# Optimization experiments

Hardware: AMD Instinct MI355X
Metric: run time of the kernel (lower is better)

Reference implementation:

```python
import jax, jax.numpy as jnp
import numpy as np
import math

D = 256
NH = 4
MULT = 128
N = MULT * D // NH  # 8192
N_LAYER = 6
VOCAB = 256
THETA = 2 ** 16
EPS = 1e-5


def get_freqs(n):
    ar = jnp.arange(n, dtype=jnp.float32)
    q = jnp.floor(ar / 2.0) * 2.0  # quantize in pairs
    return 1.0 / (THETA ** (q / n)) / (2.0 * math.pi)


def layer_norm(x):
    m = jnp.mean(x, axis=-1, keepdims=True)
    v = jnp.var(x, axis=-1, keepdims=True)
    return (x - m) / jnp.sqrt(v + EPS)


def rope_apply(v, cos, sin):
    # interleaved rotation: v_rot = stack((-v[odd], v[even])) interleaved back
    v_rot = jnp.stack([-v[..., 1::2], v[..., ::2]], axis=-1).reshape(v.shape)
    return v * cos + v_rot * sin


def setup_inputs() -> dict:
    key = jax.random.key(0)
    ks = jax.random.split(key, 6)
    idx = jax.random.randint(ks[0], (1, 1024), 0, VOCAB)
    embed = jax.random.normal(ks[1], (VOCAB, D), dtype=jnp.float32) * 0.02
    encoder = jax.random.normal(ks[2], (NH, D, N), dtype=jnp.float32) * 0.02
    encoder_v = jax.random.normal(ks[3], (NH, D, N), dtype=jnp.float32) * 0.02
    decoder = jax.random.normal(ks[4], (NH * N, D), dtype=jnp.float32) * 0.02
    lm_head = jax.random.normal(ks[5], (D, VOCAB), dtype=jnp.float32) * 0.02
    return {"idx": idx, "embed": embed, "encoder": encoder,
            "encoder_v": encoder_v, "decoder": decoder, "lm_head": lm_head}


def reference(idx, embed, encoder, encoder_v, decoder, lm_head):
    B, T = idx.shape
    x = layer_norm(embed[idx])  # (B, T, D)

    freqs = get_freqs(N)  # (N,)
    phases = (jnp.arange(T, dtype=jnp.float32)[:, None] * freqs[None, :]) % 1.0
    phases = phases * (2.0 * math.pi)
    cos = jnp.cos(phases)[None, None]  # (1,1,T,N)
    sin = jnp.sin(phases)[None, None]

    causal = jnp.tril(jnp.ones((T, T), dtype=jnp.float32), k=-1)  # strict lower

    for _ in range(N_LAYER):
        # x_sparse: (B, nh, T, N)
        x_sparse = jax.nn.relu(jnp.einsum('btd,hdn->bhtn', x, encoder))
        QR = rope_apply(x_sparse, cos, sin)
        # raw (no-softmax) strictly-causal attention, V = x broadcast over heads
        scores = jnp.einsum('bhtn,bhsn->bhts', QR, QR) * causal
        yKV = layer_norm(jnp.einsum('bhts,bsd->bhtd', scores, x))
        y_sparse = jax.nn.relu(jnp.einsum('bhtd,hdn->bhtn', yKV, encoder_v))
        xy = x_sparse * y_sparse  # (B, nh, T, N)
        # head-major flatten then project back to D
        yMLP = xy.transpose(0, 2, 1, 3).reshape(B, T, NH * N) @ decoder
        y = layer_norm(yMLP)
        x = layer_norm(x + y)

    logits = x @ lm_head  # (B, T, VOCAB)
    return logits
```

## Files before the change

kernel.cpp:

```cpp
#include <hip/hip_runtime.h>
#include <math.h>


typedef __bf16 bf16;
typedef bf16  bf16x2 __attribute__((ext_vector_type(2)));
typedef bf16  bf16x8 __attribute__((ext_vector_type(8)));
typedef float f32x4  __attribute__((ext_vector_type(4)));

#define BM 128
#define BN 128
#define BK 32
#define SW 32

typedef __attribute__((address_space(3))) unsigned int lds_uint;
typedef const __attribute__((address_space(1))) unsigned int glb_uint;

__device__ __forceinline__ void ld_g2l16(const void* g, void* l) {
  __builtin_amdgcn_global_load_lds((glb_uint*)g, (lds_uint*)l, 16, 0, 0);
}

__device__ __forceinline__ float block_sum256(float v) {
  __shared__ float sb[4];
#pragma unroll
  for (int o = 32; o > 0; o >>= 1) v += __shfl_down(v, o);
  __syncthreads();
  if ((threadIdx.x & 63) == 0) sb[threadIdx.x >> 6] = v;
  __syncthreads();
  return sb[0] + sb[1] + sb[2] + sb[3];
}

template <int MODE>
__global__ __launch_bounds__(256) void gemm_bt(
    const bf16* __restrict__ A, long lda, long aZ, long aZ2,
    const bf16* __restrict__ Bt, long ldb, long bZ, long bZ2,
    void* __restrict__ Cv, long ldc, long cZ,
    void* __restrict__ Dv, long dZ,
    int M, int N, int K) {
  int m0, n0;
  long z = blockIdx.z;
  if (MODE == 6) {
    const int combo = blockIdx.x;
    const int tile  = blockIdx.y;
    const int tr = (int)((sqrtf(8.f * tile + 1.f) - 1.f) * 0.5f);
    const int tc = tile - tr * (tr + 1) / 2;
    m0 = tr * BM; n0 = tc * BN;
    A  += (long)(combo >> 3) * aZ2 + (long)(combo & 7) * aZ;
    Bt += (long)(combo >> 3) * bZ2 + (long)(combo & 7) * bZ;
  } else if (MODE == 7) {
    const int combo = blockIdx.x;
    z = combo;
    m0 = (blockIdx.y >> 1) * BM;
    n0 = (blockIdx.y & 1) * BN;
    A  += (combo & 7) * aZ + (combo >> 3) * aZ2;
    Bt += (combo & 7) * bZ + (combo >> 3) * bZ2;
  } else {
    m0 = blockIdx.y * BM;
    n0 = blockIdx.x * BN;
    if (MODE == 2 && n0 > m0) return;
    A  += (z & 3) * aZ + (z >> 2) * aZ2;
    Bt += (z & 3) * bZ + (z >> 2) * bZ2;
  }

  __shared__ __align__(16) bf16 As[2][BM * SW];
  __shared__ __align__(16) bf16 Bs[2][BN * SW];

  const int tid  = threadIdx.x;
  const int lane = tid & 63;
  const int wr   = (tid >> 6) >> 1;
  const int wc   = (tid >> 6) & 1;
  const int l15  = lane & 15;
  const int qd   = lane >> 4;

  f32x4 acc[4][4] = {};

  int Keff = K;
  if (MODE == 3) { int kc = m0 + BM; Keff = kc < K ? kc : K; }

  const int srow = tid >> 2;
  const int skc  = (tid & 3) * 8;
  const bf16* ap = A + (long)(m0 + srow) * lda + skc;
  const bf16* bp = Bt + (long)(n0 + srow) * ldb + skc;

  auto stage = [&](int buf, int k0) {
    char* AsB = (char*)&As[buf][0];
    char* BsB = (char*)&Bs[buf][0];
    ld_g2l16(ap + k0,            AsB + tid * 16);
    ld_g2l16(ap + k0 + 64 * lda, AsB + 4096 + tid * 16);
    ld_g2l16(bp + k0,            BsB + tid * 16);
    ld_g2l16(bp + k0 + 64 * ldb, BsB + 4096 + tid * 16);
  };
  auto compute = [&](int buf) {
    bf16x8 af[4], bfr[4];
#pragma unroll
    for (int i = 0; i < 4; i++)
      af[i] = *(const bf16x8*)&As[buf][(wr * 64 + i * 16 + l15) * SW + qd * 8];
#pragma unroll
    for (int j = 0; j < 4; j++)
      bfr[j] = *(const bf16x8*)&Bs[buf][(wc * 64 + j * 16 + l15) * SW + qd * 8];
#pragma unroll
    for (int i = 0; i < 4; i++)
#pragma unroll
      for (int j = 0; j < 4; j++)
        acc[i][j] = __builtin_amdgcn_mfma_f32_16x16x32_bf16(af[i], bfr[j], acc[i][j], 0, 0, 0);
  };

  stage(0, 0);
  __syncthreads();
  int cur = 0;
  for (int k0 = BK; k0 < Keff; k0 += BK) {
    stage(cur ^ 1, k0);
    compute(cur);
    __syncthreads();
    cur ^= 1;
  }
  compute(cur);

#pragma unroll
  for (int i = 0; i < 4; i++) {
#pragma unroll
    for (int j = 0; j < 4; j++) {
#pragma unroll
      for (int r = 0; r < 4; r++) {
        const int row = m0 + wr * 64 + i * 16 + qd * 4 + r;
        const int col = n0 + wc * 64 + j * 16 + l15;
        float v = acc[i][j][r];
        if (MODE == 1) {
          float rv = fmaxf(v, 0.f);
          float pv = __shfl_xor(rv, 1);
          ((bf16*)Cv)[z * cZ + (long)row * ldc + col] = (bf16)rv;
          float freq = exp2f(-(float)(col >> 1) * (1.0f / 256.0f)) * 0.15915494309189535f;
          float ph = (float)row * freq;
          ph -= floorf(ph);
          float s, c;
          __sincosf(ph * 6.283185307179586f, &s, &c);
          float rot = (col & 1) ? pv : -pv;
          ((bf16*)Dv)[z * dZ + (long)row * ldc + col] = (bf16)(rv * c + rot * s);
        } else if (MODE == 2) {
          ((bf16*)Cv)[z * cZ + (long)row * ldc + col] = (bf16)((col < row) ? v : 0.f);
        } else if (MODE == 4) {
          float rv = fmaxf(v, 0.f);
          float xv = (float)((const bf16*)Dv)[z * dZ + (long)row * 8192 + col];
          ((bf16*)Cv)[z * cZ + (long)row * ldc + col] = (bf16)(rv * xv);
        } else if (MODE == 6) {
          const int combo = blockIdx.x;
          long base = (((long)(combo & 7) * 4 + (combo >> 3)) * 36 + blockIdx.y) * 16384;
          ((bf16*)Cv)[base + (long)(row - m0) * 128 + (col - n0)] = (bf16)v;
        } else {
          ((float*)Cv)[z * cZ + (long)row * ldc + col] = v;
        }
      }
    }
  }
}

__global__ void reduce_sc(const bf16* __restrict__ scpart, bf16* __restrict__ sc) {
  const int tile = blockIdx.x >> 2, q = blockIdx.x & 3, head = blockIdx.y;
  const int tr = (int)((sqrtf(8.f * tile + 1.f) - 1.f) * 0.5f);
  const int tc = tile - tr * (tr + 1) / 2;
  const long t0p = ((long)head * 589824 + (long)tile * 16384) >> 1;
  const bf16x2* sp = (const bf16x2*)scpart;
  for (int p = q * 2048 + threadIdx.x; p < q * 2048 + 2048; p += 256) {
    float s0 = 0.f, s1 = 0.f;
#pragma unroll
    for (int s = 0; s < 8; s++) {
      bf16x2 v = sp[(long)s * 1179648 + t0p + p];
      s0 += (float)v.x; s1 += (float)v.y;
    }
    int i = p * 2;
    int lr = i >> 7, lc = i & 127;
    int grow = tr * 128 + lr, gcol = tc * 128 + lc;
    bf16x2 o;
    o.x = (bf16)((gcol < grow) ? s0 : 0.f);
    o.y = (bf16)((gcol + 1 < grow) ? s1 : 0.f);
    *(bf16x2*)&sc[(long)head * 1048576 + (long)grow * 1024 + gcol] = o;
  }
}

__global__ void transpose_cvt(const float* __restrict__ in, bf16* __restrict__ out,
                              int R, int C, long inZ, long outZ) {
  in += (long)blockIdx.z * inZ;
  out += (long)blockIdx.z * outZ;
  __shared__ float tile[32][33];
  int c0 = blockIdx.x * 32, r0 = blockIdx.y * 32;
  int lc = threadIdx.x & 31, lr8 = threadIdx.x >> 5;
#pragma unroll
  for (int i = 0; i < 32; i += 8)
    tile[lr8 + i][lc] = in[(long)(r0 + lr8 + i) * C + c0 + lc];
  __syncthreads();
#pragma unroll
  for (int i = 0; i < 32; i += 8)
    out[(long)(c0 + lr8 + i) * R + r0 + lc] = (bf16)tile[lc][lr8 + i];
}

__global__ void embed_ln(const int* __restrict__ idx, const float* __restrict__ embed,
                         float* __restrict__ x, bf16* __restrict__ xb,
                         bf16* __restrict__ xT) {
  int t = blockIdx.x, d = threadIdx.x;
  float v = embed[(long)idx[t] * 256 + d];
  float m = block_sum256(v) * (1.0f / 256.0f);
  float c = v - m;
  float var = block_sum256(c * c) * (1.0f / 256.0f);
  float o = c * rsqrtf(var + 1e-5f);
  x[t * 256 + d] = o;
  xb[t * 256 + d] = (bf16)o;
  xT[d * 1024 + t] = (bf16)o;
}

__global__ void ln_rows(const float* __restrict__ in, bf16* __restrict__ out) {
  int r = blockIdx.x, d = threadIdx.x;
  float v = in[(long)r * 256 + d];
  float m = block_sum256(v) * (1.0f / 256.0f);
  float c = v - m;
  float var = block_sum256(c * c) * (1.0f / 256.0f);
  out[(long)r * 256 + d] = (bf16)(c * rsqrtf(var + 1e-5f));
}

__global__ void ln_fuse(const float* __restrict__ part, float* __restrict__ x,
                        bf16* __restrict__ xb, bf16* __restrict__ xT) {
  int t = blockIdx.x, d = threadIdx.x;
  float s = 0.f;
#pragma unroll
  for (int i = 0; i < 32; i++) s += part[(long)i * 262144 + t * 256 + d];
  float m = block_sum256(s) * (1.0f / 256.0f);
  float c = s - m;
  float var = block_sum256(c * c) * (1.0f / 256.0f);
  float y = c * rsqrtf(var + 1e-5f);
  float zv = x[t * 256 + d] + y;
  m = block_sum256(zv) * (1.0f / 256.0f);
  c = zv - m;
  var = block_sum256(c * c) * (1.0f / 256.0f);
  float o = c * rsqrtf(var + 1e-5f);
  x[t * 256 + d] = o;
  xb[t * 256 + d] = (bf16)o;
  xT[d * 1024 + t] = (bf16)o;
}

extern "C" void kernel_launch(void* const* d_in, const int* in_sizes, int n_in,
                              void* d_out, int out_size, void* d_ws, size_t ws_size,
                              hipStream_t stream) {
  const int*   idx = (const int*)d_in[0];
  const float* emb = (const float*)d_in[1];
  float* out = (float*)d_out;
  char* ws  = (char*)d_ws;

  bf16*  encT   = (bf16*)(ws + 0L);
  bf16*  encvT  = (bf16*)(ws + 16777216L);
  bf16*  decT   = (bf16*)(ws + 33554432L);
  bf16*  lmT    = (bf16*)(ws + 50331648L);
  float* x      = (float*)(ws + 50462720L);
  bf16*  xb     = (bf16*)(ws + 51511296L);
  bf16*  xT     = (bf16*)(ws + 52035584L);
  bf16*  xs     = (bf16*)(ws + 52559872L);
  bf16*  qr     = (bf16*)(ws + 119668736L);
  bf16*  sc     = (bf16*)(ws + 186777600L);
  bf16*  scpart = (bf16*)(ws + 195166208L);
  float* ykv    = (float*)(ws + 195166208L);
  bf16*  ykvln  = (bf16*)(ws + 199360512L);
  float* part   = (float*)(ws + 195166208L);
  const bool big = ws_size >= 232914944UL;

  transpose_cvt<<<dim3(256, 8, 4), dim3(256), 0, stream>>>((const float*)d_in[2], encT, 256, 8192, 2097152L, 2097152L);
  transpose_cvt<<<dim3(256, 8, 4), dim3(256), 0, stream>>>((const float*)d_in[3], encvT, 256, 8192, 2097152L, 2097152L);
  transpose_cvt<<<dim3(8, 1024, 1), dim3(256), 0, stream>>>((const float*)d_in[4], decT, 32768, 256, 0L, 0L);
  transpose_cvt<<<dim3(8, 8, 1), dim3(256), 0, stream>>>((const float*)d_in[5], lmT, 256, 256, 0L, 0L);
  embed_ln<<<dim3(1024), dim3(256), 0, stream>>>(idx, emb, x, xb, xT);

  for (int l = 0; l < 6; l++) {
    gemm_bt<1><<<dim3(64, 8, 4), dim3(256), 0, stream>>>(
        xb, 256L, 0L, 0L, encT, 256L, 2097152L, 8388608L,
        (void*)xs, 8192L, 8388608L, (void*)qr, 8388608L, 1024, 8192, 256);
    if (big) {
      gemm_bt<6><<<dim3(32, 36), dim3(256), 0, stream>>>(
          qr, 8192L, 1024L, 8388608L, qr, 8192L, 1024L, 8388608L,
          (void*)scpart, 0L, 0L, (void*)0, 0L, 1024, 1024, 1024);
      reduce_sc<<<dim3(144, 4), dim3(256), 0, stream>>>(scpart, sc);
    } else {
      gemm_bt<2><<<dim3(8, 8, 4), dim3(256), 0, stream>>>(
          qr, 8192L, 8388608L, 33554432L, qr, 8192L, 8388608L, 33554432L,
          (void*)sc, 1024L, 1048576L, (void*)0, 0L, 1024, 1024, 8192);
    }
    gemm_bt<3><<<dim3(2, 8, 4), dim3(256), 0, stream>>>(
        sc, 1024L, 1048576L, 4194304L, xT, 1024L, 0L, 0L,
        (void*)ykv, 256L, 262144L, (void*)0, 0L, 1024, 256, 1024);
    ln_rows<<<dim3(4096), dim3(256), 0, stream>>>(ykv, ykvln);
    gemm_bt<4><<<dim3(64, 8, 4), dim3(256), 0, stream>>>(
        ykvln, 256L, 262144L, 1048576L, encvT, 256L, 2097152L, 8388608L,
        (void*)qr, 8192L, 8388608L, (void*)xs, 8388608L, 1024, 8192, 256);
    gemm_bt<7><<<dim3(32, 16), dim3(256), 0, stream>>>(
        qr, 8192L, 1024L, 8388608L, decT, 32768L, 1024L, 8192L,
        (void*)part, 256L, 262144L, (void*)0, 0L, 1024, 256, 1024);
    ln_fuse<<<dim3(1024), dim3(256), 0, stream>>>(part, x, xb, xT);
  }
  gemm_bt<5><<<dim3(2, 8, 1), dim3(256), 0, stream>>>(
      xb, 256L, 0L, 0L, lmT, 256L, 0L, 0L,
      (void*)out, 256L, 0L, (void*)0, 0L, 1024, 256, 256);
}
```

Baseline: 1.473 ms.

## Use 256x256 tiles with 512 threads for split-K causal score GEMM

Replaces the 128x128-tile split-K score kernel (1152 blocks over 36 lower-triangular tiles per head/slice) with a dedicated 256x256-tile kernel covering 10 triangular super-tiles per head/slice using 8 waves. Each wave computes a 128x64 subtile, and subtiles strictly above the diagonal skip their store, so the output layout stays compatible with reduce_sc. Larger tiles raise arithmetic intensity and halve the global/LDS loads per FLOP. The cost is extra wasted MFMA work on the diagonal super-tiles, far fewer blocks (320), and higher register pressure from 32 accumulators per thread.

```diff
diff --git a/kernel.cpp b/kernel.cpp
--- a/kernel.cpp
+++ b/kernel.cpp
@@ -38,15 +38,7 @@
     int M, int N, int K) {
   int m0, n0;
   long z = blockIdx.z;
-  if (MODE == 6) {
-    const int combo = blockIdx.x;
-    const int tile  = blockIdx.y;
-    const int tr = (int)((sqrtf(8.f * tile + 1.f) - 1.f) * 0.5f);
-    const int tc = tile - tr * (tr + 1) / 2;
-    m0 = tr * BM; n0 = tc * BN;
-    A  += (long)(combo >> 3) * aZ2 + (long)(combo & 7) * aZ;
-    Bt += (long)(combo >> 3) * bZ2 + (long)(combo & 7) * bZ;
-  } else if (MODE == 7) {
+  if (MODE == 7) {
     const int combo = blockIdx.x;
     z = combo;
     m0 = (blockIdx.y >> 1) * BM;
@@ -141,13 +133,91 @@
           float rv = fmaxf(v, 0.f);
           float xv = (float)((const bf16*)Dv)[z * dZ + (long)row * 8192 + col];
           ((bf16*)Cv)[z * cZ + (long)row * ldc + col] = (bf16)(rv * xv);
-        } else if (MODE == 6) {
-          const int combo = blockIdx.x;
-          long base = (((long)(combo & 7) * 4 + (combo >> 3)) * 36 + blockIdx.y) * 16384;
-          ((bf16*)Cv)[base + (long)(row - m0) * 128 + (col - n0)] = (bf16)v;
         } else {
           ((float*)Cv)[z * cZ + (long)row * ldc + col] = v;
         }
+      }
+    }
+  }
+}
+
+__global__ __launch_bounds__(512, 2) void gemm_sc256(
+    const bf16* __restrict__ QR, bf16* __restrict__ scpart) {
+  const int wgid  = blockIdx.x;
+  const int slice = wgid & 7;
+  const int j     = wgid >> 3;
+  const int head  = j / 10;
+  const int tile  = j - head * 10;
+  const int tr = (int)((sqrtf(8.f * tile + 1.f) - 1.f) * 0.5f);
+  const int tc = tile - tr * (tr + 1) / 2;
+  const int m0 = tr * 256, n0 = tc * 256;
+  const bf16* Ab = QR + (long)head * 8388608 + (long)slice * 1024;
+
+  __shared__ __align__(16) bf16 As[2][256 * SW];
+  __shared__ __align__(16) bf16 Bs[2][256 * SW];
+
+  const int tid  = threadIdx.x;
+  const int lane = tid & 63;
+  const int w    = tid >> 6;
+  const int wr   = w >> 2;
+  const int wc   = w & 3;
+  const int l15  = lane & 15;
+  const int qd   = lane >> 4;
+
+  f32x4 acc[8][4] = {};
+
+  const int srow = tid >> 2;
+  const int skc  = (tid & 3) * 8;
+  const bf16* ap = Ab + (long)(m0 + srow) * 8192 + skc;
+  const bf16* bp = Ab + (long)(n0 + srow) * 8192 + skc;
+
+  auto stage = [&](int buf, int k0) {
+    char* AsB = (char*)&As[buf][0];
+    char* BsB = (char*)&Bs[buf][0];
+    ld_g2l16(ap + k0,                AsB + tid * 16);
+    ld_g2l16(ap + k0 + 128L * 8192,  AsB + 8192 + tid * 16);
+    ld_g2l16(bp + k0,                BsB + tid * 16);
+    ld_g2l16(bp + k0 + 128L * 8192,  BsB + 8192 + tid * 16);
+  };
+  auto compute = [&](int buf) {
+    bf16x8 af[8], bfr[4];
+#pragma unroll
+    for (int i = 0; i < 8; i++)
+      af[i] = *(const bf16x8*)&As[buf][(wr * 128 + i * 16 + l15) * SW + qd * 8];
+#pragma unroll
+    for (int jj = 0; jj < 4; jj++)
+      bfr[jj] = *(const bf16x8*)&Bs[buf][(wc * 64 + jj * 16 + l15) * SW + qd * 8];
+#pragma unroll
+    for (int i = 0; i < 8; i++)
+#pragma unroll
+      for (int jj = 0; jj < 4; jj++)
+        acc[i][jj] = __builtin_amdgcn_mfma_f32_16x16x32_bf16(af[i], bfr[jj], acc[i][jj], 0, 0, 0);
+  };
+
+  stage(0, 0);
+  __syncthreads();
+  int cur = 0;
+  for (int k0 = BK; k0 < 1024; k0 += BK) {
+    stage(cur ^ 1, k0);
+    compute(cur);
+    __syncthreads();
+    cur ^= 1;
+  }
+  compute(cur);
+
+  const int R = tr * 2 + wr;
+  const int C = tc * 2 + (wc >> 1);
+  if (R < C) return;
+  bf16* outp = scpart + (((long)slice * 4 + head) * 36 + (long)R * (R + 1) / 2 + C) * 16384;
+#pragma unroll
+  for (int i = 0; i < 8; i++) {
+#pragma unroll
+    for (int jj = 0; jj < 4; jj++) {
+#pragma unroll
+      for (int r = 0; r < 4; r++) {
+        const int lr = i * 16 + qd * 4 + r;
+        const int lc = (wc & 1) * 64 + jj * 16 + l15;
+        outp[(long)lr * 128 + lc] = (bf16)acc[i][jj][r];
       }
     }
   }
@@ -270,9 +340,7 @@
         xb, 256L, 0L, 0L, encT, 256L, 2097152L, 8388608L,
         (void*)xs, 8192L, 8388608L, (void*)qr, 8388608L, 1024, 8192, 256);
     if (big) {
-      gemm_bt<6><<<dim3(32, 36), dim3(256), 0, stream>>>(
-          qr, 8192L, 1024L, 8388608L, qr, 8192L, 1024L, 8388608L,
-          (void*)scpart, 0L, 0L, (void*)0, 0L, 1024, 1024, 1024);
+      gemm_sc256<<<dim3(320), dim3(512), 0, stream>>>(qr, scpart);
       reduce_sc<<<dim3(144, 4), dim3(256), 0, stream>>>(scpart, sc);
     } else {
       gemm_bt<2><<<dim3(8, 8, 4), dim3(256), 0, stream>>>(
```

Measured after the change: 1.569 ms. 6.5% more time.
